# Kernel optimization log

Measured on AMD Instinct MI355X. Metric: run time of the kernel, lower is better.

The kernel has to match this reference:

```python
import jax, jax.numpy as jnp
import numpy as np

N = 10000        # nodes
E = 320000       # edges
IN = 256         # input_dim
D = 64           # output_dim per head
H = 4            # num_heads
ED = 32          # edge_dim
T = 8            # num_etypes
SLOPE = 0.2      # leaky relu negative slope


def setup_inputs() -> dict:
    key = jax.random.key(0)
    ks = jax.random.split(key, 12)
    s = 0.05
    feat = jax.random.normal(ks[0], (N, IN), jnp.float32)
    edge_weight = jax.random.uniform(ks[1], (E,), jnp.float32)
    row = jax.random.randint(ks[2], (E,), 0, N, jnp.int32)
    col = jax.random.randint(ks[3], (E,), 0, N, jnp.int32)
    etype_idxs = jax.random.randint(ks[4], (E,), 0, T, jnp.int32)
    W = jax.random.normal(ks[5], (IN, D * H), jnp.float32) * s
    edge_emb_table = jax.random.normal(ks[6], (T, ED), jnp.float32) * s
    W_r = jax.random.normal(ks[7], (T, ED, ED * H), jnp.float32) * s
    a_l = jax.random.normal(ks[8], (H, D), jnp.float32) * s
    a_r = jax.random.normal(ks[9], (H, D), jnp.float32) * s
    a_e = jax.random.normal(ks[10], (H, ED), jnp.float32) * s
    W_res = jax.random.normal(ks[11], (IN, D * H), jnp.float32) * s
    b_res = jnp.zeros((D * H,), jnp.float32)
    return dict(feat=feat, edge_weight=edge_weight, row=row, col=col,
                etype_idxs=etype_idxs, W=W, edge_emb_table=edge_emb_table,
                W_r=W_r, a_l=a_l, a_r=a_r, a_e=a_e, W_res=W_res, b_res=b_res)


def reference(feat, edge_weight, row, col, etype_idxs, W, edge_emb_table,
              W_r, a_l, a_r, a_e, W_res, b_res):
    # node projection: [N, H, D]
    emb = jnp.nan_to_num(feat @ W).reshape(N, H, D)
    # typed linear on edge-type embeddings: only T distinct outputs, gather per edge
    type_out = jnp.einsum('ti,tio->to', edge_emb_table, W_r).reshape(T, H, ED)
    edge_e = type_out[etype_idxs]                      # [E, H, ED]
    # attention logits
    hl = jnp.einsum('nhd,hd->nh', emb, a_l)            # [N, H]
    hr = jnp.einsum('nhd,hd->nh', emb, a_r)            # [N, H]
    he = jnp.einsum('ehd,hd->eh', edge_e, a_e)         # [E, H]
    att = jax.nn.sigmoid(jax.nn.leaky_relu(hl[row] + hr[col] + he, SLOPE))
    att = att * edge_weight[:, None]                   # [E, H]
    # u_mul_e + sum scatter: src=row, dst=col
    msg = emb[row] * att[:, :, None]                   # [E, H, D]
    agg = jax.ops.segment_sum(msg, col, num_segments=N)  # [N, H, D]
    # original permutes to [N, D, H] before flattening
    out = jnp.transpose(agg, (0, 2, 1)).reshape(N, D * H)
    out = out + feat @ W_res + b_res                   # residual
    return jax.nn.elu(out)
```

## Files before the change

### kernel.cpp

```cpp
#include <hip/hip_runtime.h>
#include <hip/hip_bf16.h>
#include <math.h>

#define N_NODES 10000
#define MPAD 10112
#define N_EDGES 320000
#define IN_DIM 256
#define NH 4
#define EDIM 32
#define NT 8
#define SLOPE 0.2f
#define CAP 96

#define GB (MPAD / 64)
#define EBT 512
#define EB ((N_EDGES + EBT - 1) / EBT)

#define PREP_WT_BLOCKS 32
#define PREP_HE_BLOCKS 4
#define PREP_Z_BLOCKS 40
#define PREP_BLOCKS (PREP_WT_BLOCKS + PREP_HE_BLOCKS + PREP_Z_BLOCKS)

typedef __attribute__((ext_vector_type(8))) short short8b;
typedef __attribute__((ext_vector_type(4))) float f32x4;

__device__ __forceinline__ float bf2f(ushort u) {
  return __uint_as_float(((unsigned)u) << 16);
}
__device__ __forceinline__ ushort f2bf(float f) {
  __hip_bfloat16 h = __float2bfloat16(f);
  return *(ushort*)&h;
}
__device__ __forceinline__ unsigned pk2(float a, float b) {
  return (unsigned)f2bf(a) | ((unsigned)f2bf(b) << 16);
}

__global__ __launch_bounds__(256) void prep_kernel(
    const float* __restrict__ W, const float* __restrict__ W_res,
    const float* __restrict__ table, const float* __restrict__ W_r,
    const float* __restrict__ a_e, ushort* __restrict__ Wtb,
    float* __restrict__ he_type, int* __restrict__ cnt) {
  const int b = blockIdx.x;
  const int tid = threadIdx.x;
  if (b < PREP_WT_BLOCKS) {
    __shared__ float Ls[64][68];
    const bool isres = b >= 16;
    const float* src = isres ? W_res : W;
    const int t = b & 15;
    const int k0 = (t >> 2) * 64, c0 = (t & 3) * 64;
    {
      int r = tid >> 2, cc = (tid & 3) * 16;
      const float* sp = &src[(size_t)(k0 + r) * 256 + c0 + cc];
      float4 v0 = ((const float4*)sp)[0];
      float4 v1 = ((const float4*)sp)[1];
      float4 v2 = ((const float4*)sp)[2];
      float4 v3 = ((const float4*)sp)[3];
      *(float4*)&Ls[r][cc + 0] = v0;
      *(float4*)&Ls[r][cc + 4] = v1;
      *(float4*)&Ls[r][cc + 8] = v2;
      *(float4*)&Ls[r][cc + 12] = v3;
    }
    __syncthreads();
    {
      int cloc = tid >> 2, kc = (tid & 3) * 16;
      int csrc = c0 + cloc;
      int cdst = isres ? (256 + csrc) : (((csrc & 63) << 2) | (csrc >> 6));
      unsigned u[8];
#pragma unroll
      for (int q = 0; q < 8; ++q)
        u[q] = pk2(Ls[kc + 2 * q][cloc], Ls[kc + 2 * q + 1][cloc]);
      uint4 w0 = make_uint4(u[0], u[1], u[2], u[3]);
      uint4 w1 = make_uint4(u[4], u[5], u[6], u[7]);
      *(uint4*)&Wtb[(size_t)cdst * 256 + k0 + kc] = w0;
      *(uint4*)&Wtb[(size_t)cdst * 256 + k0 + kc + 8] = w1;
    }
  } else if (b < PREP_WT_BLOCKS + PREP_HE_BLOCKS) {
    int t2 = (b - PREP_WT_BLOCKS) * 256 + tid;
    int t = t2 >> 7, h = (t2 >> 5) & 3, d = t2 & 31;
    float acc = 0.f;
    for (int q = 0; q < EDIM; ++q)
      acc += table[t * EDIM + q] * W_r[(t * EDIM + q) * (EDIM * NH) + h * EDIM + d];
    acc *= a_e[h * EDIM + d];
#pragma unroll
    for (int o = 16; o; o >>= 1) acc += __shfl_xor(acc, o, 32);
    if (d == 0) he_type[t * NH + h] = acc;
  } else {
    int z = (b - PREP_WT_BLOCKS - PREP_HE_BLOCKS) * 256 + tid;
    if (z <= N_NODES) cnt[z] = 0;
  }
}

__global__ __launch_bounds__(512) void gemm_bucket_kernel(
    const float* __restrict__ feat, const ushort* __restrict__ Wtb,
    const float* __restrict__ b_res,
    const float* __restrict__ a_l, const float* __restrict__ a_r,
    ushort* __restrict__ emb_t, ushort* __restrict__ resb,
    float* __restrict__ hl, float* __restrict__ hr,
    const int* __restrict__ row, const int* __restrict__ colv,
    const int* __restrict__ et, const float* __restrict__ ew,
    int* cnt, uint2* __restrict__ slots) {
  __shared__ ushort As[64 * 256];
  const int tid = threadIdx.x;

  if (blockIdx.x >= GB) {
    int e = (blockIdx.x - GB) * EBT + tid;
    if (e < N_EDGES) {
      int r = row[e], c = colv[e], t = et[e];
      float w = ew[e];
      uint2 slot;
      slot.x = ((unsigned)t << 16) | (unsigned)r;
      slot.y = __float_as_uint(w);
      int s = atomicAdd(&cnt[c], 1);
      if (s < CAP) slots[(size_t)c * CAP + s] = slot;
    }
    return;
  }

  const int rowbase = blockIdx.x * 64;

#pragma unroll
  for (int i = 0; i < 4; ++i) {
    int c = tid + i * 512;
    int rowl = c >> 5, slot = c & 31;
    int gr = rowbase + rowl;
    uint4 pk = make_uint4(0, 0, 0, 0);
    if (gr < N_NODES) {
      float4 x = *(const float4*)&feat[(size_t)gr * 256 + slot * 8];
      float4 y = *(const float4*)&feat[(size_t)gr * 256 + slot * 8 + 4];
      pk.x = pk2(x.x, x.y); pk.y = pk2(x.z, x.w);
      pk.z = pk2(y.x, y.y); pk.w = pk2(y.z, y.w);
    }
    int idx = rowl * 256 + (((slot * 16) ^ ((rowl & 7) << 4)) >> 1);
    *(uint4*)&As[idx] = pk;
  }
  __syncthreads();

  const int wave = tid >> 6, lane = tid & 63;
  const int col0 = wave * 64;
  const int lr = lane & 15;
  const int lkq = lane >> 4;
  f32x4 acc[4][4] = {};
  const ushort* Bb = Wtb + (size_t)(col0 + lr) * 256 + lkq * 8;

#pragma unroll
  for (int ks = 0; ks < 8; ++ks) {
    short8b a[4], b[4];
#pragma unroll
    for (int m = 0; m < 4; ++m) {
      int rowl = m * 16 + lr;
      int kb = ks * 64 + lkq * 16;
      int idx = rowl * 256 + ((kb ^ ((rowl & 7) << 4)) >> 1);
      a[m] = *(const short8b*)&As[idx];
    }
#pragma unroll
    for (int n = 0; n < 4; ++n)
      b[n] = *(const short8b*)(Bb + (size_t)(n * 16) * 256 + ks * 32);
#pragma unroll
    for (int n = 0; n < 4; ++n)
#pragma unroll
      for (int m = 0; m < 4; ++m)
        acc[n][m] = __builtin_amdgcn_mfma_f32_16x16x32_bf16(b[n], a[m], acc[n][m], 0, 0, 0);
  }

  __syncthreads();
  float* PL = (float*)As;
  float* PR = PL + 1024;

  if (col0 < 256) {
#pragma unroll
    for (int m = 0; m < 4; ++m) {
      const int r = rowbase + m * 16 + lr;
      if (r < N_NODES) {
#pragma unroll
        for (int n = 0; n < 4; ++n) {
          int d = (col0 >> 2) + n * 4 + lkq;
          ushort4 pk4;
          pk4.x = f2bf(acc[n][m][0]); pk4.y = f2bf(acc[n][m][1]);
          pk4.z = f2bf(acc[n][m][2]); pk4.w = f2bf(acc[n][m][3]);
          *(ushort4*)&emb_t[((size_t)r * 64 + d) * 4] = pk4;
        }
      }
      float pl[4] = {0.f, 0.f, 0.f, 0.f}, pr[4] = {0.f, 0.f, 0.f, 0.f};
#pragma unroll
      for (int n = 0; n < 4; ++n) {
        int d = (col0 >> 2) + n * 4 + lkq;
#pragma unroll
        for (int h = 0; h < 4; ++h) {
          pl[h] = fmaf(acc[n][m][h], a_l[h * 64 + d], pl[h]);
          pr[h] = fmaf(acc[n][m][h], a_r[h * 64 + d], pr[h]);
        }
      }
#pragma unroll
      for (int h = 0; h < 4; ++h) {
        pl[h] += __shfl_xor(pl[h], 16);
        pl[h] += __shfl_xor(pl[h], 32);
        pr[h] += __shfl_xor(pr[h], 16);
        pr[h] += __shfl_xor(pr[h], 32);
      }
      if (lkq == 0) {
#pragma unroll
        for (int h = 0; h < 4; ++h) {
          PL[(wave * 64 + m * 16 + lr) * 4 + h] = pl[h];
          PR[(wave * 64 + m * 16 + lr) * 4 + h] = pr[h];
        }
      }
    }
  } else {
#pragma unroll
    for (int m = 0; m < 4; ++m) {
      const int r = rowbase + m * 16 + lr;
      if (r < N_NODES) {
#pragma unroll
        for (int n = 0; n < 4; ++n) {
          int c = (col0 - 256) + n * 16 + lkq * 4;
          float4 br = *(const float4*)&b_res[c];
          ushort4 pk4;
          pk4.x = f2bf(acc[n][m][0] + br.x); pk4.y = f2bf(acc[n][m][1] + br.y);
          pk4.z = f2bf(acc[n][m][2] + br.z); pk4.w = f2bf(acc[n][m][3] + br.w);
          *(ushort4*)&resb[(size_t)r * 256 + c] = pk4;
        }
      }
    }
  }

  __syncthreads();
  if (tid < 128) {
    int rl = tid >> 1, sel = tid & 1;
    const float* P = sel ? PR : PL;
    float4 v;
    v.x = P[rl * 4 + 0] + P[256 + rl * 4 + 0] + P[512 + rl * 4 + 0] + P[768 + rl * 4 + 0];
    v.y = P[rl * 4 + 1] + P[256 + rl * 4 + 1] + P[512 + rl * 4 + 1] + P[768 + rl * 4 + 1];
    v.z = P[rl * 4 + 2] + P[256 + rl * 4 + 2] + P[512 + rl * 4 + 2] + P[768 + rl * 4 + 2];
    v.w = P[rl * 4 + 3] + P[256 + rl * 4 + 3] + P[512 + rl * 4 + 3] + P[768 + rl * 4 + 3];
    int gr = rowbase + rl;
    if (gr < N_NODES) *(float4*)&(sel ? hr : hl)[gr * 4] = v;
  }
}

__global__ __launch_bounds__(256) void agg_kernel(
    const int* __restrict__ cnt, const uint2* __restrict__ slots,
    const float* __restrict__ hl, const float* __restrict__ hr,
    const float* __restrict__ he_type,
    const ushort* __restrict__ emb_t, const ushort* __restrict__ resb,
    float* __restrict__ out) {
  __shared__ uint4 meta[4 * CAP];
  const int wv = threadIdx.x >> 6;
  const int lane = threadIdx.x & 63;
  const int nu = __builtin_amdgcn_readfirstlane(blockIdx.x * 4 + wv);
  const int cn = min(cnt[nu], CAP);

  {
    float4 R = *(const float4*)&hr[nu * 4];
    for (int j = lane; j < cn; j += 64) {
      uint2 s = slots[(size_t)nu * CAP + j];
      int src = s.x & 0xffff, t = s.x >> 16;
      float w = __uint_as_float(s.y);
      float4 L = *(const float4*)&hl[src * 4];
      float4 He = *(const float4*)&he_type[t * 4];
      float x[4] = {L.x + R.x + He.x, L.y + R.y + He.y,
                    L.z + R.z + He.z, L.w + R.w + He.w};
      float a[4];
#pragma unroll
      for (int h = 0; h < 4; ++h) {
        float v = x[h];
        v = v >= 0.f ? v : SLOPE * v;
        a[h] = w / (1.f + __expf(-v));
      }
      uint4 m;
      m.x = pk2(a[0], a[1]);
      m.y = pk2(a[2], a[3]);
      m.z = (unsigned)src;
      m.w = 0;
      meta[wv * CAP + j] = m;
    }
  }
  __builtin_amdgcn_wave_barrier();

  float acc0 = 0.f, acc1 = 0.f, acc2 = 0.f, acc3 = 0.f;
  const uint4* mb = &meta[wv * CAP];

#define AGG_FMA(V, WA, WB)                                      \
  acc0 = fmaf(bf2f((V).x), __uint_as_float((WA) << 16), acc0);  \
  acc1 = fmaf(bf2f((V).y), __uint_as_float((WA) & 0xffff0000u), acc1); \
  acc2 = fmaf(bf2f((V).z), __uint_as_float((WB) << 16), acc2);  \
  acc3 = fmaf(bf2f((V).w), __uint_as_float((WB) & 0xffff0000u), acc3);

  const int j4 = cn & ~3;
#pragma unroll 2
  for (int j = 0; j < j4; j += 4) {
    uint4 m0 = mb[j], m1 = mb[j + 1], m2 = mb[j + 2], m3 = mb[j + 3];
    ushort4 v0 = *(const ushort4*)&emb_t[((size_t)m0.z * 64 + lane) * 4];
    ushort4 v1 = *(const ushort4*)&emb_t[((size_t)m1.z * 64 + lane) * 4];
    ushort4 v2 = *(const ushort4*)&emb_t[((size_t)m2.z * 64 + lane) * 4];
    ushort4 v3 = *(const ushort4*)&emb_t[((size_t)m3.z * 64 + lane) * 4];
    AGG_FMA(v0, m0.x, m0.y)
    AGG_FMA(v1, m1.x, m1.y)
    AGG_FMA(v2, m2.x, m2.y)
    AGG_FMA(v3, m3.x, m3.y)
  }
  for (int j = j4; j < cn; ++j) {
    uint4 m0 = mb[j];
    ushort4 v0 = *(const ushort4*)&emb_t[((size_t)m0.z * 64 + lane) * 4];
    AGG_FMA(v0, m0.x, m0.y)
  }
#undef AGG_FMA

  ushort4 r4 = *(const ushort4*)&resb[((size_t)nu * 64 + lane) * 4];
  float v0 = acc0 + bf2f(r4.x), v1 = acc1 + bf2f(r4.y);
  float v2 = acc2 + bf2f(r4.z), v3 = acc3 + bf2f(r4.w);
  float4 o;
  o.x = v0 > 0.f ? v0 : expm1f(v0);
  o.y = v1 > 0.f ? v1 : expm1f(v1);
  o.z = v2 > 0.f ? v2 : expm1f(v2);
  o.w = v3 > 0.f ? v3 : expm1f(v3);
  *(float4*)&out[((size_t)nu * 64 + lane) * 4] = o;
}

extern "C" void kernel_launch(void* const* d_in, const int* in_sizes, int n_in,
                              void* d_out, int out_size, void* d_ws, size_t ws_size,
                              hipStream_t stream) {
  const float* feat = (const float*)d_in[0];
  const float* ew = (const float*)d_in[1];
  const int* row = (const int*)d_in[2];
  const int* col = (const int*)d_in[3];
  const int* etype = (const int*)d_in[4];
  const float* W = (const float*)d_in[5];
  const float* table = (const float*)d_in[6];
  const float* W_r = (const float*)d_in[7];
  const float* a_l = (const float*)d_in[8];
  const float* a_r = (const float*)d_in[9];
  const float* a_e = (const float*)d_in[10];
  const float* W_res = (const float*)d_in[11];
  const float* b_res = (const float*)d_in[12];
  float* out = (float*)d_out;

  char* w = (char*)d_ws;
  auto alloc = [&](size_t bytes) {
    char* pp = w;
    w += (bytes + 255) & ~(size_t)255;
    return pp;
  };
  ushort* Wtb = (ushort*)alloc((size_t)512 * 256 * 2);
  ushort* emb_t = (ushort*)alloc((size_t)N_NODES * 256 * 2);
  ushort* resb = (ushort*)alloc((size_t)N_NODES * 256 * 2);
  uint2* slots = (uint2*)alloc((size_t)N_NODES * CAP * 8);
  float* hl = (float*)alloc((size_t)N_NODES * NH * 4);
  float* hr = (float*)alloc((size_t)N_NODES * NH * 4);
  float* he_type = (float*)alloc(NT * NH * 4);
  int* cnt = (int*)alloc((size_t)(N_NODES + 1) * 4);

  prep_kernel<<<PREP_BLOCKS, 256, 0, stream>>>(W, W_res, table, W_r, a_e,
                                               Wtb, he_type, cnt);
  gemm_bucket_kernel<<<GB + EB, 512, 0, stream>>>(
      feat, Wtb, b_res, a_l, a_r, emb_t, resb, hl, hr,
      row, col, etype, ew, cnt, slots);
  agg_kernel<<<N_NODES / 4, 256, 0, stream>>>(cnt, slots, hl, hr, he_type,
                                              emb_t, resb, out);
}
```

Before: 51.83 us.

## Split wave into two half-waves gathering 16-byte rows per edge in aggregation

The aggregation loop now has each half of the wave process a different edge. Each lane loads a 16-byte uint4 (8 bf16 values) instead of 8 bytes, so one wave covers two source rows per load instruction. The two half-wave partial sums are combined with a cross-lane shuffle, and the edge list is zero-padded to a multiple of four so the scalar tail loop can go. This is meant to cut the number of gather instructions and improve per-lane load width. In exchange it adds shuffles, doubles the accumulator registers, and leaves half the lanes idle during the epilogue.

Result: no change. 51.28 us (-1.1%).

```diff
diff --git a/kernel.cpp b/kernel.cpp
--- a/kernel.cpp
+++ b/kernel.cpp
@@ -26,6 +26,12 @@
 
 __device__ __forceinline__ float bf2f(ushort u) {
   return __uint_as_float(((unsigned)u) << 16);
+}
+__device__ __forceinline__ float blo(unsigned u) {
+  return __uint_as_float(u << 16);
+}
+__device__ __forceinline__ float bhi(unsigned u) {
+  return __uint_as_float(u & 0xffff0000u);
 }
 __device__ __forceinline__ ushort f2bf(float f) {
   __hip_bfloat16 h = __float2bfloat16(f);
@@ -248,6 +254,7 @@
   const int lane = threadIdx.x & 63;
   const int nu = __builtin_amdgcn_readfirstlane(blockIdx.x * 4 + wv);
   const int cn = min(cnt[nu], CAP);
+  const int cn4 = (cn + 3) & ~3;
 
   {
     float4 R = *(const float4*)&hr[nu * 4];
@@ -273,47 +280,62 @@
       m.w = 0;
       meta[wv * CAP + j] = m;
     }
+    for (int j = cn + lane; j < cn4; j += 64)
+      meta[wv * CAP + j] = make_uint4(0, 0, 0, 0);
   }
   __builtin_amdgcn_wave_barrier();
 
-  float acc0 = 0.f, acc1 = 0.f, acc2 = 0.f, acc3 = 0.f;
+  const int eh = lane >> 5;
+  const int dp = lane & 31;
+  float a00 = 0.f, a01 = 0.f, a02 = 0.f, a03 = 0.f;
+  float a10 = 0.f, a11 = 0.f, a12 = 0.f, a13 = 0.f;
   const uint4* mb = &meta[wv * CAP];
 
-#define AGG_FMA(V, WA, WB)                                      \
-  acc0 = fmaf(bf2f((V).x), __uint_as_float((WA) << 16), acc0);  \
-  acc1 = fmaf(bf2f((V).y), __uint_as_float((WA) & 0xffff0000u), acc1); \
-  acc2 = fmaf(bf2f((V).z), __uint_as_float((WB) << 16), acc2);  \
-  acc3 = fmaf(bf2f((V).w), __uint_as_float((WB) & 0xffff0000u), acc3);
-
-  const int j4 = cn & ~3;
+#define AGG_FMA2(V, WA, WB)                      \
+  a00 = fmaf(blo((V).x), blo(WA), a00);          \
+  a01 = fmaf(bhi((V).x), bhi(WA), a01);          \
+  a02 = fmaf(blo((V).y), blo(WB), a02);          \
+  a03 = fmaf(bhi((V).y), bhi(WB), a03);          \
+  a10 = fmaf(blo((V).z), blo(WA), a10);          \
+  a11 = fmaf(bhi((V).z), bhi(WA), a11);          \
+  a12 = fmaf(blo((V).w), blo(WB), a12);          \
+  a13 = fmaf(bhi((V).w), bhi(WB), a13);
+
 #pragma unroll 2
-  for (int j = 0; j < j4; j += 4) {
-    uint4 m0 = mb[j], m1 = mb[j + 1], m2 = mb[j + 2], m3 = mb[j + 3];
-    ushort4 v0 = *(const ushort4*)&emb_t[((size_t)m0.z * 64 + lane) * 4];
-    ushort4 v1 = *(const ushort4*)&emb_t[((size_t)m1.z * 64 + lane) * 4];
-    ushort4 v2 = *(const ushort4*)&emb_t[((size_t)m2.z * 64 + lane) * 4];
-    ushort4 v3 = *(const ushort4*)&emb_t[((size_t)m3.z * 64 + lane) * 4];
-    AGG_FMA(v0, m0.x, m0.y)
-    AGG_FMA(v1, m1.x, m1.y)
-    AGG_FMA(v2, m2.x, m2.y)
-    AGG_FMA(v3, m3.x, m3.y)
-  }
-  for (int j = j4; j < cn; ++j) {
-    uint4 m0 = mb[j];
-    ushort4 v0 = *(const ushort4*)&emb_t[((size_t)m0.z * 64 + lane) * 4];
-    AGG_FMA(v0, m0.x, m0.y)
-  }
-#undef AGG_FMA
-
-  ushort4 r4 = *(const ushort4*)&resb[((size_t)nu * 64 + lane) * 4];
-  float v0 = acc0 + bf2f(r4.x), v1 = acc1 + bf2f(r4.y);
-  float v2 = acc2 + bf2f(r4.z), v3 = acc3 + bf2f(r4.w);
-  float4 o;
-  o.x = v0 > 0.f ? v0 : expm1f(v0);
-  o.y = v1 > 0.f ? v1 : expm1f(v1);
-  o.z = v2 > 0.f ? v2 : expm1f(v2);
-  o.w = v3 > 0.f ? v3 : expm1f(v3);
-  *(float4*)&out[((size_t)nu * 64 + lane) * 4] = o;
+  for (int j = 0; j < cn4; j += 4) {
+    uint4 m0 = mb[j + eh];
+    uint4 m1 = mb[j + 2 + eh];
+    uint4 v0 = *(const uint4*)&emb_t[((size_t)m0.z * 64 + dp * 2) * 4];
+    uint4 v1 = *(const uint4*)&emb_t[((size_t)m1.z * 64 + dp * 2) * 4];
+    AGG_FMA2(v0, m0.x, m0.y)
+    AGG_FMA2(v1, m1.x, m1.y)
+  }
+#undef AGG_FMA2
+
+  a00 += __shfl_xor(a00, 32); a01 += __shfl_xor(a01, 32);
+  a02 += __shfl_xor(a02, 32); a03 += __shfl_xor(a03, 32);
+  a10 += __shfl_xor(a10, 32); a11 += __shfl_xor(a11, 32);
+  a12 += __shfl_xor(a12, 32); a13 += __shfl_xor(a13, 32);
+
+  if (lane < 32) {
+    uint4 r4 = *(const uint4*)&resb[((size_t)nu * 64 + dp * 2) * 4];
+    float v00 = a00 + blo(r4.x), v01 = a01 + bhi(r4.x);
+    float v02 = a02 + blo(r4.y), v03 = a03 + bhi(r4.y);
+    float v10 = a10 + blo(r4.z), v11 = a11 + bhi(r4.z);
+    float v12 = a12 + blo(r4.w), v13 = a13 + bhi(r4.w);
+    float4 o0, o1;
+    o0.x = v00 > 0.f ? v00 : expm1f(v00);
+    o0.y = v01 > 0.f ? v01 : expm1f(v01);
+    o0.z = v02 > 0.f ? v02 : expm1f(v02);
+    o0.w = v03 > 0.f ? v03 : expm1f(v03);
+    o1.x = v10 > 0.f ? v10 : expm1f(v10);
+    o1.y = v11 > 0.f ? v11 : expm1f(v11);
+    o1.z = v12 > 0.f ? v12 : expm1f(v12);
+    o1.w = v13 > 0.f ? v13 : expm1f(v13);
+    float* op = &out[((size_t)nu * 64 + dp * 2) * 4];
+    *(float4*)op = o0;
+    *(float4*)(op + 4) = o1;
+  }
 }
 
 extern "C" void kernel_launch(void* const* d_in, const int* in_sizes, int n_in,
```
